# Performance work log

Measured on AMD Instinct MI355X. Metric: run time of the kernel, lower is better.

## Reference

```python
import jax, jax.numpy as jnp
import numpy as np
from jax import lax

B, N, C = 4, 16384, 384
HEADS, HD = 8, 48
ALPHA = 4.0
KS = 5
HH = WW = 128


def setup_inputs() -> dict:
    key = jax.random.key(0)
    ks = jax.random.split(key, 9)
    s = 0.02
    return {
        "x": jax.random.normal(ks[0], (B, N, C), jnp.float32),
        "W_qg": jax.random.normal(ks[1], (C, 2 * C), jnp.float32) * s,
        "W_kv": jax.random.normal(ks[2], (C, 2 * C), jnp.float32) * s,
        "W_proj": jax.random.normal(ks[3], (C, C), jnp.float32) * s,
        "b_proj": jnp.zeros((C,), jnp.float32),
        "pos_enc": jax.random.normal(ks[4], (1, N, C), jnp.float32) * 0.02,
        "power_p": jax.random.normal(ks[5], (1, HEADS, 1, HD), jnp.float32) * 0.5,
        "scale_p": jax.random.normal(ks[6], (1, 1, C), jnp.float32) * 0.5,
        "dwc_w": jax.random.normal(ks[7], (HD, 1, KS, KS), jnp.float32) * s,
        "dwc_b": jnp.zeros((HD,), jnp.float32),
        "H": HH,
        "W": WW,
    }


def _relu_pow(x, p):
    # relu(x) ** p with safe gradients at x <= 0
    r = jax.nn.relu(x)
    base = jnp.where(r > 0, r, 1.0)
    return jnp.where(r > 0, base ** p, 0.0)


def reference(x, W_qg, W_kv, W_proj, b_proj, pos_enc, power_p, scale_p, dwc_w, dwc_b, H, W):
    Bx, Nx, Cx = x.shape
    h = power_p.shape[1]
    hd = power_p.shape[-1]

    qg = x @ W_qg                      # [B,N,2C]
    q, g = qg[..., :Cx], qg[..., Cx:]
    kv = x @ W_kv                      # [B,N,2C] (sr_ratio == 1)
    k, v = kv[..., :Cx], kv[..., Cx:]
    n = Nx
    k = k + pos_enc

    scale = jax.nn.softplus(scale_p)            # [1,1,C]
    power = 1.0 + ALPHA * jax.nn.sigmoid(power_p)  # [1,h,1,hd]
    q = q / scale
    k = k / scale

    # [B,h,N,hd]
    q = q.reshape(Bx, Nx, h, hd).transpose(0, 2, 1, 3)
    k = k.reshape(Bx, n, h, hd).transpose(0, 2, 1, 3)
    v = v.reshape(Bx, n, h, hd).transpose(0, 2, 1, 3)

    q_pos = _relu_pow(q, power)
    q_neg = _relu_pow(-q, power)
    k_pos = _relu_pow(k, power)
    k_neg = _relu_pow(-k, power)

    q_sim = jnp.concatenate([q_pos, q_neg], axis=-1)   # [B,h,N,2hd]
    q_opp = jnp.concatenate([q_neg, q_pos], axis=-1)
    kk = jnp.concatenate([k_pos, k_neg], axis=-1)      # [B,h,n,2hd]
    v1, v2 = v[..., : hd // 2], v[..., hd // 2:]

    k_mean = kk.mean(axis=2, keepdims=True)            # [B,h,1,2hd]
    inv_n = 1.0 / n

    z_sim = 1.0 / (jnp.sum(q_sim * k_mean, axis=-1, keepdims=True) + 1e-6)
    kv1 = jnp.einsum('bhnd,bhne->bhde', kk, v1) * inv_n  # [B,h,2hd,hd/2]
    x_sim = jnp.einsum('bhnd,bhde->bhne', q_sim, kv1) * z_sim

    z_opp = 1.0 / (jnp.sum(q_opp * k_mean, axis=-1, keepdims=True) + 1e-6)
    kv2 = jnp.einsum('bhnd,bhne->bhde', kk, v2) * inv_n
    x_opp = jnp.einsum('bhnd,bhde->bhne', q_opp, kv2) * z_opp

    out = jnp.concatenate([x_sim, x_opp], axis=-1)     # [B,h,N,hd]
    out = out.transpose(0, 2, 1, 3).reshape(Bx, Nx, Cx)

    # depthwise conv gate on v
    v4 = v.reshape(Bx * h, H, W, hd).transpose(0, 3, 1, 2)  # [B*h, hd, H, W]
    vc = lax.conv_general_dilated(
        v4, dwc_w, window_strides=(1, 1), padding='SAME',
        feature_group_count=hd,
        dimension_numbers=('NCHW', 'OIHW', 'NCHW'))
    vc = vc + dwc_b[None, :, None, None]
    v_out = vc.reshape(Bx, Cx, Nx).transpose(0, 2, 1)  # [B,N,C]

    out = (out + v_out) * g
    out = out @ W_proj + b_proj
    return out
```

## Files before the change

### kernel.cpp

```cpp
#include <hip/hip_runtime.h>
#include <math.h>


#define NB 4
#define NTOK 16384
#define CDIM 384
#define NHEAD 8
#define HDIM 48
#define IMGH 128
#define IMGW 128

typedef unsigned short u16;
typedef unsigned int u32;
typedef __attribute__((ext_vector_type(8))) short bf16x8;
typedef __attribute__((ext_vector_type(4))) float f32x4;

__device__ __forceinline__ float bf2f(u16 u) {
  return __uint_as_float(((unsigned)u) << 16);
}
__device__ __forceinline__ u16 f2bf(float f) {
  unsigned u = __float_as_uint(f);
  u += 0x7FFF + ((u >> 16) & 1);
  return (u16)(u >> 16);
}
__device__ __forceinline__ float pow_mag(float r, float p) {
  if (r < 1e-20f) return 0.0f;
  return exp2f(fminf(p * log2f(r), 80.0f));
}
__device__ __forceinline__ float ldx1(const void* p, size_t i, bool f32) {
  return f32 ? ((const float*)p)[i] : bf2f(((const u16*)p)[i]);
}
__device__ __forceinline__ void gload16(u16* lds, const u16* g) {
  __builtin_amdgcn_global_load_lds(
      (const __attribute__((address_space(1))) u32*)g,
      (__attribute__((address_space(3))) u32*)lds, 16, 0, 0);
}

__global__ __launch_bounds__(256) void k0_detect(const void* __restrict__ x,
                                                 int* __restrict__ flag) {
  __shared__ int s[256];
  const u16* p = (const u16*)x;
  const int t = threadIdx.x;
  int good = 0;
#pragma unroll
  for (int i = 0; i < 16; ++i) {
    const u16 w = p[t * 16 + i];
    const int e = (w >> 7) & 0xFF;
    good += (e >= 0x60 && e <= 0x85) ? 1 : 0;
  }
  s[t] = good;
  __syncthreads();
  for (int o = 128; o > 0; o >>= 1) {
    if (t < o) s[t] += s[t + o];
    __syncthreads();
  }
  if (t == 0) *flag = (s[0] >= (4096 * 4) / 5) ? 0 : 1;
}

__global__ __launch_bounds__(256) void kx_convert(const void* __restrict__ x,
                                                  const int* __restrict__ flag,
                                                  u16* __restrict__ xbf) {
  if (*flag == 0) return;
  const size_t S = (size_t)NB * NTOK * CDIM;
  const size_t tid = (size_t)blockIdx.x * 256 + threadIdx.x;
  const size_t stride = (size_t)gridDim.x * 256;
  const float4* xf = (const float4*)x;
  for (size_t i = tid; i < S / 8; i += stride) {
    const float4 a = xf[i * 2 + 0];
    const float4 b = xf[i * 2 + 1];
    *(ushort4*)(xbf + i * 8 + 0) = make_ushort4(f2bf(a.x), f2bf(a.y), f2bf(a.z), f2bf(a.w));
    *(ushort4*)(xbf + i * 8 + 4) = make_ushort4(f2bf(b.x), f2bf(b.y), f2bf(b.z), f2bf(b.w));
  }
}

__global__ __launch_bounds__(256) void kprep(
    const void* __restrict__ Wqg, const void* __restrict__ Wkv,
    const void* __restrict__ Wp, const int* __restrict__ flag,
    u16* __restrict__ W2T, u16* __restrict__ WpT)
{
  const bool f32 = (*flag != 0);
  const int idx = blockIdx.x * 256 + threadIdx.x;
  if (idx < 1536 * 384) {
    const int n = idx / 384, k = idx - n * 384;
    const float v = (n < 768) ? ldx1(Wqg, (size_t)k * 768 + n, f32)
                              : ldx1(Wkv, (size_t)k * 768 + (n - 768), f32);
    W2T[idx] = f2bf(v);
  } else {
    const int j = idx - 1536 * 384;
    if (j < 384 * 384) {
      const int n = j / 384, k = j - n * 384;
      WpT[j] = f2bf(ldx1(Wp, (size_t)k * 384 + n, f32));
    }
  }
}

__global__ __launch_bounds__(512) void k1_mfma(
    const void* __restrict__ x, const u16* __restrict__ xbf,
    const u16* __restrict__ W2T,
    const void* __restrict__ pos_enc, const void* __restrict__ scale_p,
    const int* __restrict__ flag, const int conv_ok,
    u16* __restrict__ qsT, u16* __restrict__ gT, u16* __restrict__ ksT, u16* __restrict__ vT)
{
  const bool f32 = (*flag != 0);
  const bool fast = (!f32) || (conv_ok != 0);
  const u16* Asrc = f32 ? xbf : (const u16*)x;
  __shared__ __align__(16) u16 smem[17408];
  u16* Asm = smem;
  u16* Bsm = smem + 8192;
  const int t = threadIdx.x;
  const int bid = blockIdx.x;
  const int rm = (bid & 7) * 768 + (bid >> 3);
  const int m_idx = rm / 12;
  const int n_idx = rm - m_idx * 12;
  const int n0 = n_idx * 128;
  const int m0 = m_idx * 128;
  const int wave = t >> 6, lane = t & 63;
  const int wr = wave >> 2, wc = wave & 3;
  const int lm = lane & 15, lq = lane >> 4;

  f32x4 acc[4][2] = {};

  auto STAGE = [&](int k0) {
#pragma unroll
    for (int i = 0; i < 2; ++i) {
      const int chunk = i * 512 + t;
      const int row = chunk >> 3, c8 = chunk & 7;
      const int sc8 = c8 ^ (row & 7);
      u16* lpA = &Asm[(i * 512 + wave * 64) * 8];
      u16* lpB = &Bsm[(i * 512 + wave * 64) * 8];
      gload16(lpA, Asrc + (size_t)(m0 + row) * CDIM + k0 + sc8 * 8);
      gload16(lpB, W2T + (size_t)(n0 + row) * CDIM + k0 + sc8 * 8);
    }
  };
  auto COMPUTE = [&]() {
#pragma unroll
    for (int kh = 0; kh < 2; ++kh) {
      bf16x8 af[4], bfr[2];
#pragma unroll
      for (int r = 0; r < 4; ++r) {
        const int row = wr * 64 + r * 16 + lm;
        af[r] = *(const bf16x8*)&Asm[row * 64 + (((kh * 4 + lq) ^ (row & 7)) * 8)];
      }
#pragma unroll
      for (int cb = 0; cb < 2; ++cb) {
        const int row = wc * 32 + cb * 16 + lm;
        bfr[cb] = *(const bf16x8*)&Bsm[row * 64 + (((kh * 4 + lq) ^ (row & 7)) * 8)];
      }
#pragma unroll
      for (int r = 0; r < 4; ++r)
#pragma unroll
        for (int cb = 0; cb < 2; ++cb)
          acc[r][cb] = __builtin_amdgcn_mfma_f32_16x16x32_bf16(af[r], bfr[cb], acc[r][cb], 0, 0, 0);
    }
  };

  if (fast) {
    for (int ks = 0; ks < 6; ++ks) {
      STAGE(ks * 64);
      __syncthreads();
      COMPUTE();
      __syncthreads();
    }
  } else {
    for (int k0 = 0; k0 < CDIM; k0 += 64) {
#pragma unroll
      for (int i = 0; i < 2; ++i) {
        const int chunk = t + i * 512;
        const int row = chunk >> 3, c8 = chunk & 7;
        const int ldsoff = row * 64 + ((c8 ^ (row & 7)) * 8);
        const float* xp = (const float*)x + (size_t)(m0 + row) * CDIM + k0 + c8 * 8;
        const float4 v0 = *(const float4*)xp;
        const float4 v1 = *(const float4*)(xp + 4);
        *(ushort4*)&Asm[ldsoff]     = make_ushort4(f2bf(v0.x), f2bf(v0.y), f2bf(v0.z), f2bf(v0.w));
        *(ushort4*)&Asm[ldsoff + 4] = make_ushort4(f2bf(v1.x), f2bf(v1.y), f2bf(v1.z), f2bf(v1.w));
        *(uint4*)&Bsm[ldsoff] = *(const uint4*)(W2T + (size_t)(n0 + row) * CDIM + k0 + c8 * 8);
      }
      __syncthreads();
      COMPUTE();
      __syncthreads();
    }
  }

  u16* et = smem;
  const int b = m0 >> 14;
  const int TOK0 = m0 & (NTOK - 1);
  const int region = n0 / CDIM;
#pragma unroll
  for (int cb = 0; cb < 2; ++cb) {
    const int cl = wc * 32 + cb * 16 + lm;
    const int c = (n0 - region * CDIM) + cl;
    float inv = 1.0f;
    if (region == 0 || region == 2) inv = 1.0f / log1pf(expf(ldx1(scale_p, c, f32)));
#pragma unroll
    for (int r = 0; r < 4; ++r) {
      const int tl = wr * 64 + r * 16 + lq * 4;
      const f32x4 v = acc[r][cb];
      ushort4 w;
      if (region == 2) {
        const int tok = TOK0 + tl;
        const float p0 = ldx1(pos_enc, (size_t)(tok + 0) * CDIM + c, f32);
        const float p1 = ldx1(pos_enc, (size_t)(tok + 1) * CDIM + c, f32);
        const float p2 = ldx1(pos_enc, (size_t)(tok + 2) * CDIM + c, f32);
        const float p3 = ldx1(pos_enc, (size_t)(tok + 3) * CDIM + c, f32);
        w = make_ushort4(f2bf((v[0] + p0) * inv), f2bf((v[1] + p1) * inv),
                         f2bf((v[2] + p2) * inv), f2bf((v[3] + p3) * inv));
      } else if (region == 0) {
        w = make_ushort4(f2bf(v[0] * inv), f2bf(v[1] * inv), f2bf(v[2] * inv), f2bf(v[3] * inv));
      } else {
        w = make_ushort4(f2bf(v[0]), f2bf(v[1]), f2bf(v[2]), f2bf(v[3]));
      }
      *(ushort4*)&et[cl * 136 + tl] = w;
    }
  }
  __syncthreads();
  u16* dst = (region == 0) ? qsT : (region == 1) ? gT : (region == 2) ? ksT : vT;
  const int cbase = b * CDIM + (n0 - region * CDIM);
#pragma unroll
  for (int i = 0; i < 4; ++i) {
    const int idx = i * 512 + t;
    const int row = idx >> 4, seg = idx & 15;
    const uint4 val = *(const uint4*)&et[row * 136 + seg * 8];
    *(uint4*)(dst + ((size_t)(cbase + row)) * NTOK + TOK0 + seg * 8) = val;
  }
}

__global__ __launch_bounds__(256) void k2_stats(
    const u16* __restrict__ ksT, const u16* __restrict__ vT,
    const void* __restrict__ power_p, const int* __restrict__ flag,
    float* __restrict__ km, float* __restrict__ kvm)
{
  const bool f32 = (*flag != 0);
  __shared__ __align__(16) u16 kkL[96][72];
  __shared__ __align__(16) u16 vL[48][72];
  __shared__ float pw[48];
  const int bh = blockIdx.x;
  const int b = bh >> 3, h = bh & 7;
  const int t = threadIdx.x;
  if (t < 48) pw[t] = 1.0f + 4.0f / (1.0f + expf(-ldx1(power_p, h * HDIM + t, f32)));
  __syncthreads();
  const int wave = t >> 6, lane = t & 63;
  const int lm = lane & 15, lq = lane >> 4;
  f32x4 acc[2][3] = {};
  float ksum = 0.0f;
  const u16* ksbase = ksT + ((size_t)(b * CDIM + h * HDIM)) * NTOK;
  const u16* vbase  = vT  + ((size_t)(b * CDIM + h * HDIM)) * NTOK;
  const int n0base = blockIdx.y * 1024;
  for (int tile = 0; tile < 16; ++tile) {
    const int n0 = n0base + tile * 64;
    for (int i = t; i < 48 * 16; i += 256) {
      const int c = i >> 4, qd = (i & 15) * 4;
      ushort4 kq = *(const ushort4*)(ksbase + (size_t)c * NTOK + n0 + qd);
      ushort4 vq = *(const ushort4*)(vbase  + (size_t)c * NTOK + n0 + qd);
      const float p = pw[c];
      float kf[4] = {bf2f(kq.x), bf2f(kq.y), bf2f(kq.z), bf2f(kq.w)};
      ushort4 pos, neg;
#pragma unroll
      for (int jj = 0; jj < 4; ++jj) {
        const float f = pow_mag(fabsf(kf[jj]), p);
        ((u16*)&pos)[jj] = f2bf((kf[jj] > 0.f) ? f : 0.f);
        ((u16*)&neg)[jj] = f2bf((kf[jj] < 0.f) ? f : 0.f);
      }
      *(ushort4*)&kkL[c][qd]      = pos;
      *(ushort4*)&kkL[c + 48][qd] = neg;
      *(ushort4*)&vL[c][qd]       = vq;
    }
    __syncthreads();
    if (wave < 3) {
      const int mbase = wave * 32;
#pragma unroll
      for (int kh = 0; kh < 2; ++kh) {
        bf16x8 af[2], bfr[3];
#pragma unroll
        for (int mi = 0; mi < 2; ++mi)
          af[mi] = *(const bf16x8*)&kkL[mbase + mi * 16 + lm][kh * 32 + lq * 8];
#pragma unroll
        for (int nj = 0; nj < 3; ++nj)
          bfr[nj] = *(const bf16x8*)&vL[nj * 16 + lm][kh * 32 + lq * 8];
#pragma unroll
        for (int mi = 0; mi < 2; ++mi)
#pragma unroll
          for (int nj = 0; nj < 3; ++nj)
            acc[mi][nj] = __builtin_amdgcn_mfma_f32_16x16x32_bf16(af[mi], bfr[nj], acc[mi][nj], 0, 0, 0);
      }
    }
    if (t < 96) {
#pragma unroll
      for (int nn = 0; nn < 64; nn += 4) {
        const ushort4 kq4 = *(const ushort4*)&kkL[t][nn];
        ksum += (bf2f(kq4.x) + bf2f(kq4.y)) + (bf2f(kq4.z) + bf2f(kq4.w));
      }
    }
    __syncthreads();
  }
  const float inv_n = 1.0f / (float)NTOK;
  if (wave < 3) {
    const int mbase = wave * 32;
#pragma unroll
    for (int mi = 0; mi < 2; ++mi)
#pragma unroll
      for (int nj = 0; nj < 3; ++nj) {
        const f32x4 v = acc[mi][nj];
#pragma unroll
        for (int reg = 0; reg < 4; ++reg) {
          const int d = mbase + mi * 16 + lq * 4 + reg;
          const int e = nj * 16 + lm;
          atomicAdd(&kvm[(size_t)bh * 96 * 48 + d * 48 + e], v[reg] * inv_n);
        }
      }
  }
  if (t < 96) atomicAdd(&km[bh * 96 + t], ksum * inv_n);
}

__global__ __launch_bounds__(256) void k3_attn(
    const u16* __restrict__ qsT, u16* __restrict__ attnT,
    const float* __restrict__ km_g, const float* __restrict__ kvm_g,
    const void* __restrict__ power_p, const int* __restrict__ flag)
{
  const bool f32 = (*flag != 0);
  __shared__ __align__(16) float kvmL[96][48];
  __shared__ float kmL[96];
  __shared__ float pw[48];
  const int bh = blockIdx.y;
  const int b = bh >> 3, h = bh & 7;
  const int t = threadIdx.x;
  for (int i = t; i < 96 * 48; i += 256) kvmL[i / 48][i % 48] = kvm_g[(size_t)bh * 96 * 48 + i];
  if (t < 96) kmL[t] = km_g[bh * 96 + t];
  if (t < 48) pw[t] = 1.0f + 4.0f / (1.0f + expf(-ldx1(power_p, h * HDIM + t, f32)));
  __syncthreads();
  const int n = blockIdx.x * 512 + t;
  const size_t chan0 = ((size_t)(b * CDIM + h * HDIM)) * NTOK + n;
  const u16* qbase = qsT + chan0;
  u16* obase = attnT + chan0;
  float4 accs[2][6] = {}, acco[2][6] = {};
  float zs[2] = {}, zo[2] = {};
  for (int d = 0; d < 48; ++d) {
    const float p = pw[d];
    float qp[2], qn[2];
#pragma unroll
    for (int i = 0; i < 2; ++i) {
      const float qv = bf2f(qbase[(size_t)d * NTOK + i * 256]);
      const float f = pow_mag(fabsf(qv), p);
      qp[i] = (qv > 0.f) ? f : 0.f;
      qn[i] = (qv < 0.f) ? f : 0.f;
      zs[i] = fmaf(qp[i], kmL[d], zs[i]); zs[i] = fmaf(qn[i], kmL[d + 48], zs[i]);
      zo[i] = fmaf(qn[i], kmL[d], zo[i]); zo[i] = fmaf(qp[i], kmL[d + 48], zo[i]);
    }
#pragma unroll
    for (int e4 = 0; e4 < 6; ++e4) {
      const float4 kvA = *(const float4*)&kvmL[d][e4 * 4];
      const float4 kvB = *(const float4*)&kvmL[d + 48][e4 * 4];
      const float4 kvC = *(const float4*)&kvmL[d][24 + e4 * 4];
      const float4 kvD = *(const float4*)&kvmL[d + 48][24 + e4 * 4];
#pragma unroll
      for (int i = 0; i < 2; ++i) {
        accs[i][e4].x = fmaf(qp[i], kvA.x, fmaf(qn[i], kvB.x, accs[i][e4].x));
        accs[i][e4].y = fmaf(qp[i], kvA.y, fmaf(qn[i], kvB.y, accs[i][e4].y));
        accs[i][e4].z = fmaf(qp[i], kvA.z, fmaf(qn[i], kvB.z, accs[i][e4].z));
        accs[i][e4].w = fmaf(qp[i], kvA.w, fmaf(qn[i], kvB.w, accs[i][e4].w));
        acco[i][e4].x = fmaf(qn[i], kvC.x, fmaf(qp[i], kvD.x, acco[i][e4].x));
        acco[i][e4].y = fmaf(qn[i], kvC.y, fmaf(qp[i], kvD.y, acco[i][e4].y));
        acco[i][e4].z = fmaf(qn[i], kvC.z, fmaf(qp[i], kvD.z, acco[i][e4].z));
        acco[i][e4].w = fmaf(qn[i], kvC.w, fmaf(qp[i], kvD.w, acco[i][e4].w));
      }
    }
  }
#pragma unroll
  for (int i = 0; i < 2; ++i) {
    const float zsi = 1.0f / (zs[i] + 1e-6f);
    const float zoi = 1.0f / (zo[i] + 1e-6f);
#pragma unroll
    for (int e4 = 0; e4 < 6; ++e4) {
      const float4 s = accs[i][e4], o = acco[i][e4];
      obase[(size_t)(e4 * 4 + 0) * NTOK + i * 256]    = f2bf(s.x * zsi);
      obase[(size_t)(e4 * 4 + 1) * NTOK + i * 256]    = f2bf(s.y * zsi);
      obase[(size_t)(e4 * 4 + 2) * NTOK + i * 256]    = f2bf(s.z * zsi);
      obase[(size_t)(e4 * 4 + 3) * NTOK + i * 256]    = f2bf(s.w * zsi);
      obase[(size_t)(24 + e4 * 4 + 0) * NTOK + i * 256] = f2bf(o.x * zoi);
      obase[(size_t)(24 + e4 * 4 + 1) * NTOK + i * 256] = f2bf(o.y * zoi);
      obase[(size_t)(24 + e4 * 4 + 2) * NTOK + i * 256] = f2bf(o.z * zoi);
      obase[(size_t)(24 + e4 * 4 + 3) * NTOK + i * 256] = f2bf(o.w * zoi);
    }
  }
}

__global__ __launch_bounds__(256) void k4_conv_combine(
    const u16* __restrict__ vT, const u16* __restrict__ gT,
    const void* __restrict__ dwc_w, const void* __restrict__ dwc_b,
    const int* __restrict__ flag,
    u16* __restrict__ attnT)
{
  const bool f32 = (*flag != 0);
  __shared__ float tile[20][136];
  const int bc = blockIdx.y;
  const int y0 = blockIdx.x * 16;
  const int t = threadIdx.x;
  const int d = bc % 48;
  float w[25];
#pragma unroll
  for (int i = 0; i < 25; ++i) w[i] = ldx1(dwc_w, d * 25 + i, f32);
  const float bias = ldx1(dwc_b, d, f32);
  const u16* vimg = vT + (size_t)bc * NTOK;
  for (int i = t; i < 20 * 34; i += 256) {
    const int r = i / 34, cq = (i - r * 34) * 4;
    const int gy = y0 + r - 2;
    float4 v4 = make_float4(0.f, 0.f, 0.f, 0.f);
    if (gy >= 0 && gy < IMGH) {
      const int gx0 = cq - 4;
      if (gx0 >= 0 && gx0 + 3 < IMGW) {
        const ushort4 u = *(const ushort4*)(vimg + gy * IMGW + gx0);
        v4 = make_float4(bf2f(u.x), bf2f(u.y), bf2f(u.z), bf2f(u.w));
      } else {
#pragma unroll
        for (int jj = 0; jj < 4; ++jj) {
          const int gx = gx0 + jj;
          ((float*)&v4)[jj] = (gx >= 0 && gx < IMGW) ? bf2f(vimg[gy * IMGW + gx]) : 0.f;
        }
      }
    }
    *(float4*)&tile[r][cq] = v4;
  }
  __syncthreads();
  u16* abase = attnT + (size_t)bc * NTOK;
  const u16* gbase = gT + (size_t)bc * NTOK;
#pragma unroll
  for (int pass = 0; pass < 2; ++pass) {
    const int yy = pass * 8 + (t >> 5);
    const int x0 = (t & 31) * 4;
    float a0 = bias, a1 = bias, a2 = bias, a3 = bias;
#pragma unroll
    for (int dy = 0; dy < 5; ++dy) {
      const float* row = &tile[yy + dy][0];
      const float4 A = *(const float4*)&row[x0];
      const float4 B = *(const float4*)&row[x0 + 4];
      const float4 C = *(const float4*)&row[x0 + 8];
      const float c0 = A.z, c1 = A.w, c2 = B.x, c3 = B.y,
                  c4 = B.z, c5 = B.w, c6 = C.x, c7 = C.y;
      const float w0 = w[dy * 5 + 0], w1 = w[dy * 5 + 1], w2 = w[dy * 5 + 2],
                  w3 = w[dy * 5 + 3], w4 = w[dy * 5 + 4];
      a0 = fmaf(w0, c0, fmaf(w1, c1, fmaf(w2, c2, fmaf(w3, c3, fmaf(w4, c4, a0)))));
      a1 = fmaf(w0, c1, fmaf(w1, c2, fmaf(w2, c3, fmaf(w3, c4, fmaf(w4, c5, a1)))));
      a2 = fmaf(w0, c2, fmaf(w1, c3, fmaf(w2, c4, fmaf(w3, c5, fmaf(w4, c6, a2)))));
      a3 = fmaf(w0, c3, fmaf(w1, c4, fmaf(w2, c5, fmaf(w3, c6, fmaf(w4, c7, a3)))));
    }
    const int gidx = (y0 + yy) * IMGW + x0;
    const ushort4 at = *(const ushort4*)(abase + gidx);
    const ushort4 gg = *(const ushort4*)(gbase + gidx);
    *(ushort4*)(abase + gidx) = make_ushort4(
        f2bf((bf2f(at.x) + a0) * bf2f(gg.x)),
        f2bf((bf2f(at.y) + a1) * bf2f(gg.y)),
        f2bf((bf2f(at.z) + a2) * bf2f(gg.z)),
        f2bf((bf2f(at.w) + a3) * bf2f(gg.w)));
  }
}

__global__ __launch_bounds__(256) void k4b_transpose(
    const u16* __restrict__ src,
    u16* __restrict__ dst)
{
  __shared__ u16 tile[64][68];
  const int b  = blockIdx.z;
  const int c0 = blockIdx.y * 64;
  const int n0 = blockIdx.x * 64;
  const int t = threadIdx.x;
  const int tr = t >> 4, tq = t & 15;
#pragma unroll
  for (int i = 0; i < 4; ++i) {
    const int r = tr + i * 16;
    *(ushort4*)&tile[r][tq * 4] =
        *(const ushort4*)(src + ((size_t)(b * CDIM + c0 + r)) * NTOK + n0 + tq * 4);
  }
  __syncthreads();
#pragma unroll
  for (int i = 0; i < 4; ++i) {
    const int n = tr + i * 16;
    const ushort4 vv = make_ushort4(tile[tq * 4 + 0][n], tile[tq * 4 + 1][n],
                                    tile[tq * 4 + 2][n], tile[tq * 4 + 3][n]);
    *(ushort4*)(dst + ((size_t)(b * NTOK + n0 + n)) * CDIM + c0 + tq * 4) = vv;
  }
}

__global__ __launch_bounds__(256) void k5_mfma(
    const u16* __restrict__ A,
    const u16* __restrict__ WpT,
    const void* __restrict__ bp, const int* __restrict__ flag,
    void* __restrict__ out)
{
  const bool f32 = (*flag != 0);
  __shared__ __align__(16) u16 smem[32768];
  u16* Asm0 = smem;
  u16* Asm1 = smem + 8192;
  u16* Bsm0 = smem + 16384;
  u16* Bsm1 = smem + 24576;
  const int t = threadIdx.x;
  const int bid = blockIdx.x;
  const int rm = (bid & 7) * 192 + (bid >> 3);
  const int m_idx = rm / 3;
  const int n_idx = rm - m_idx * 3;
  const int n0 = n_idx * 128;
  const int m0 = m_idx * 128;
  const int wave = t >> 6, lane = t & 63;
  const int wr = wave >> 1, wc = wave & 1;
  const int lm = lane & 15, lq = lane >> 4;

  f32x4 acc[4][4] = {};

  auto STAGE = [&](int buf, int k0) {
    u16* Ab = buf ? Asm1 : Asm0;
    u16* Bb = buf ? Bsm1 : Bsm0;
#pragma unroll
    for (int i = 0; i < 4; ++i) {
      const int chunk = i * 256 + t;
      const int row = chunk >> 3, c8 = chunk & 7;
      const int sc8 = c8 ^ (row & 7);
      u16* lpA = &Ab[(i * 256 + wave * 64) * 8];
      u16* lpB = &Bb[(i * 256 + wave * 64) * 8];
      gload16(lpA, A + (size_t)(m0 + row) * CDIM + k0 + sc8 * 8);
      gload16(lpB, WpT + (size_t)(n0 + row) * CDIM + k0 + sc8 * 8);
    }
  };
  auto COMPUTE = [&](int buf) {
    u16* Ab = buf ? Asm1 : Asm0;
    u16* Bb = buf ? Bsm1 : Bsm0;
#pragma unroll
    for (int kh = 0; kh < 2; ++kh) {
      bf16x8 af[4], bfr[4];
#pragma unroll
      for (int r = 0; r < 4; ++r) {
        const int row = wr * 64 + r * 16 + lm;
        af[r] = *(const bf16x8*)&Ab[row * 64 + (((kh * 4 + lq) ^ (row & 7)) * 8)];
      }
#pragma unroll
      for (int cb = 0; cb < 4; ++cb) {
        const int row = wc * 64 + cb * 16 + lm;
        bfr[cb] = *(const bf16x8*)&Bb[row * 64 + (((kh * 4 + lq) ^ (row & 7)) * 8)];
      }
#pragma unroll
      for (int r = 0; r < 4; ++r)
#pragma unroll
        for (int cb = 0; cb < 4; ++cb)
          acc[r][cb] = __builtin_amdgcn_mfma_f32_16x16x32_bf16(af[r], bfr[cb], acc[r][cb], 0, 0, 0);
    }
  };

  STAGE(0, 0);
  asm volatile("s_waitcnt vmcnt(0)" ::: "memory");
  __builtin_amdgcn_sched_barrier(0);
  __builtin_amdgcn_s_barrier();
  int cur = 0;
#pragma unroll
  for (int ks = 0; ks < 5; ++ks) {
    STAGE(cur ^ 1, (ks + 1) * 64);
    COMPUTE(cur);
    asm volatile("s_waitcnt vmcnt(0)" ::: "memory");
    __builtin_amdgcn_sched_barrier(0);
    __builtin_amdgcn_s_barrier();
    cur ^= 1;
  }
  COMPUTE(cur);

  if (f32) {
    float* ef = (float*)smem;
    float bb[4];
#pragma unroll
    for (int cb = 0; cb < 4; ++cb) bb[cb] = ((const float*)bp)[n0 + wc * 64 + cb * 16 + lm];
    for (int h = 0; h < 2; ++h) {
      __syncthreads();
      if (wr == h) {
#pragma unroll
        for (int cb = 0; cb < 4; ++cb) {
          const int cl = wc * 64 + cb * 16 + lm;
#pragma unroll
          for (int r = 0; r < 4; ++r) {
            const int tl = r * 16 + lq * 4;
            const f32x4 v = acc[r][cb];
#pragma unroll
            for (int reg = 0; reg < 4; ++reg)
              ef[(tl + reg) * 132 + cl] = v[reg] + bb[cb];
          }
        }
      }
      __syncthreads();
      float* ob = (float*)out + (size_t)(m0 + h * 64) * CDIM + n0;
#pragma unroll
      for (int i = 0; i < 8; ++i) {
        const int idx = i * 256 + t;
        const int row = idx >> 5, seg = idx & 31;
        const float4 val = *(const float4*)&ef[row * 132 + seg * 4];
        *(float4*)(ob + (size_t)row * CDIM + seg * 4) = val;
      }
    }
  } else {
#pragma unroll
    for (int cb = 0; cb < 4; ++cb) {
      const int cg = n0 + wc * 64 + cb * 16 + lm;
      const float bbs = bf2f(((const u16*)bp)[cg]);
#pragma unroll
      for (int r = 0; r < 4; ++r) {
        const int rowtok = m0 + wr * 64 + r * 16 + lq * 4;
        const f32x4 v = acc[r][cb];
#pragma unroll
        for (int reg = 0; reg < 4; ++reg) {
          const size_t o = (size_t)(rowtok + reg) * CDIM + cg;
          ((u16*)out)[o] = f2bf(v[reg] + bbs);
        }
      }
    }
  }
}

extern "C" void kernel_launch(void* const* d_in, const int* in_sizes, int n_in,
                              void* d_out, int out_size, void* d_ws, size_t ws_size,
                              hipStream_t stream) {
  const void* x       = d_in[0];
  const void* Wqg     = d_in[1];
  const void* Wkv     = d_in[2];
  const void* Wproj   = d_in[3];
  const void* bproj   = d_in[4];
  const void* pos_enc = d_in[5];
  const void* power_p = d_in[6];
  const void* scale_p = d_in[7];
  const void* dwc_w   = d_in[8];
  const void* dwc_b   = d_in[9];

  const size_t S = (size_t)NB * NTOK * CDIM;
  const size_t stats_off   = 256;
  const size_t stats_bytes = (size_t)(32 * 96 + 32 * 96 * 48) * sizeof(float);
  const size_t w2t_elems = 1536 * 384, wpt_elems = 384 * 384;
  const size_t need = stats_off + stats_bytes + 3 * S * sizeof(u16)
                    + (w2t_elems + wpt_elems) * sizeof(u16);
  if (ws_size < need) return;

  int*   flag = (int*)d_ws;
  float* km   = (float*)((char*)d_ws + stats_off);
  float* kvm  = km + 32 * 96;
  u16* qsT = (u16*)((char*)d_ws + stats_off + stats_bytes);
  u16* gT  = qsT + S;
  u16* ksT = gT + S;
  u16* W2T = ksT + S;
  u16* WpT = W2T + w2t_elems;
  u16* vT  = (u16*)d_out;

  const int conv_ok = (out_size >= (int)(S * 4)) ? 1 : 0;
  u16* xbf = conv_ok ? ((u16*)d_out + S) : (u16*)d_out;

  hipMemsetAsync(km, 0, stats_bytes, stream);

  k0_detect<<<1, 256, 0, stream>>>(x, flag);
  if (conv_ok) kx_convert<<<2048, 256, 0, stream>>>(x, flag, xbf);
  kprep<<<(int)((w2t_elems + wpt_elems + 255) / 256), 256, 0, stream>>>(
      Wqg, Wkv, Wproj, flag, W2T, WpT);
  k1_mfma<<<6144, 512, 0, stream>>>(x, xbf, W2T, pos_enc, scale_p, flag, conv_ok,
                                    qsT, gT, ksT, vT);
  k2_stats<<<dim3(32, 16), 256, 0, stream>>>(ksT, vT, power_p, flag, km, kvm);
  k3_attn<<<dim3(32, 32), 256, 0, stream>>>(qsT, ksT, km, kvm, power_p, flag);
  k4_conv_combine<<<dim3(8, 1536), 256, 0, stream>>>(vT, gT, dwc_w, dwc_b, flag, ksT);
  k4b_transpose<<<dim3(256, 6, 4), 256, 0, stream>>>(ksT, qsT);
  k5_mfma<<<1536, 256, 0, stream>>>(qsT, WpT, bproj, flag, d_out);
}
```

Measured before the change: 667.7 us.

## Restructure projection GEMM to 512 threads with single-buffered LDS

The final projection GEMM kernel now runs 8 waves per 128x128 tile instead of 4, each wave covering a 64x32 sub-tile, which halves the accumulator registers per thread. The LDS double buffer is dropped for a single buffer with plain __syncthreads around each k-step, cutting shared memory per block roughly in half. The aim is higher occupancy and more latency hiding across waves. The cost is that loads no longer overlap with MFMA inside a block, and every k-step now waits on two barriers.

Result: no change. 662.9 us (-0.7%).

```diff
diff --git a/kernel.cpp b/kernel.cpp
--- a/kernel.cpp
+++ b/kernel.cpp
@@ -479,18 +479,16 @@
   }
 }
 
-__global__ __launch_bounds__(256) void k5_mfma(
+__global__ __launch_bounds__(512) void k5_mfma(
     const u16* __restrict__ A,
     const u16* __restrict__ WpT,
     const void* __restrict__ bp, const int* __restrict__ flag,
     void* __restrict__ out)
 {
   const bool f32 = (*flag != 0);
-  __shared__ __align__(16) u16 smem[32768];
-  u16* Asm0 = smem;
-  u16* Asm1 = smem + 8192;
-  u16* Bsm0 = smem + 16384;
-  u16* Bsm1 = smem + 24576;
+  __shared__ __align__(16) u16 smem[17408];
+  u16* Asm = smem;
+  u16* Bsm = smem + 8192;
   const int t = threadIdx.x;
   const int bid = blockIdx.x;
   const int rm = (bid & 7) * 192 + (bid >> 3);
@@ -499,76 +497,63 @@
   const int n0 = n_idx * 128;
   const int m0 = m_idx * 128;
   const int wave = t >> 6, lane = t & 63;
-  const int wr = wave >> 1, wc = wave & 1;
+  const int wr = wave >> 2, wc = wave & 3;
   const int lm = lane & 15, lq = lane >> 4;
 
-  f32x4 acc[4][4] = {};
-
-  auto STAGE = [&](int buf, int k0) {
-    u16* Ab = buf ? Asm1 : Asm0;
-    u16* Bb = buf ? Bsm1 : Bsm0;
-#pragma unroll
-    for (int i = 0; i < 4; ++i) {
-      const int chunk = i * 256 + t;
+  f32x4 acc[4][2] = {};
+
+  auto STAGE = [&](int k0) {
+#pragma unroll
+    for (int i = 0; i < 2; ++i) {
+      const int chunk = i * 512 + t;
       const int row = chunk >> 3, c8 = chunk & 7;
       const int sc8 = c8 ^ (row & 7);
-      u16* lpA = &Ab[(i * 256 + wave * 64) * 8];
-      u16* lpB = &Bb[(i * 256 + wave * 64) * 8];
+      u16* lpA = &Asm[(i * 512 + wave * 64) * 8];
+      u16* lpB = &Bsm[(i * 512 + wave * 64) * 8];
       gload16(lpA, A + (size_t)(m0 + row) * CDIM + k0 + sc8 * 8);
       gload16(lpB, WpT + (size_t)(n0 + row) * CDIM + k0 + sc8 * 8);
     }
   };
-  auto COMPUTE = [&](int buf) {
-    u16* Ab = buf ? Asm1 : Asm0;
-    u16* Bb = buf ? Bsm1 : Bsm0;
+  auto COMPUTE = [&]() {
 #pragma unroll
     for (int kh = 0; kh < 2; ++kh) {
-      bf16x8 af[4], bfr[4];
+      bf16x8 af[4], bfr[2];
 #pragma unroll
       for (int r = 0; r < 4; ++r) {
         const int row = wr * 64 + r * 16 + lm;
-        af[r] = *(const bf16x8*)&Ab[row * 64 + (((kh * 4 + lq) ^ (row & 7)) * 8)];
-      }
-#pragma unroll
-      for (int cb = 0; cb < 4; ++cb) {
-        const int row = wc * 64 + cb * 16 + lm;
-        bfr[cb] = *(const bf16x8*)&Bb[row * 64 + (((kh * 4 + lq) ^ (row & 7)) * 8)];
+        af[r] = *(const bf16x8*)&Asm[row * 64 + (((kh * 4 + lq) ^ (row & 7)) * 8)];
+      }
+#pragma unroll
+      for (int cb = 0; cb < 2; ++cb) {
+        const int row = wc * 32 + cb * 16 + lm;
+        bfr[cb] = *(const bf16x8*)&Bsm[row * 64 + (((kh * 4 + lq) ^ (row & 7)) * 8)];
       }
 #pragma unroll
       for (int r = 0; r < 4; ++r)
 #pragma unroll
-        for (int cb = 0; cb < 4; ++cb)
+        for (int cb = 0; cb < 2; ++cb)
           acc[r][cb] = __builtin_amdgcn_mfma_f32_16x16x32_bf16(af[r], bfr[cb], acc[r][cb], 0, 0, 0);
     }
   };
 
-  STAGE(0, 0);
-  asm volatile("s_waitcnt vmcnt(0)" ::: "memory");
-  __builtin_amdgcn_sched_barrier(0);
-  __builtin_amdgcn_s_barrier();
-  int cur = 0;
-#pragma unroll
-  for (int ks = 0; ks < 5; ++ks) {
-    STAGE(cur ^ 1, (ks + 1) * 64);
-    COMPUTE(cur);
-    asm volatile("s_waitcnt vmcnt(0)" ::: "memory");
-    __builtin_amdgcn_sched_barrier(0);
-    __builtin_amdgcn_s_barrier();
-    cur ^= 1;
-  }
-  COMPUTE(cur);
+  for (int ks = 0; ks < 6; ++ks) {
+    STAGE(ks * 64);
+    __syncthreads();
+    COMPUTE();
+    __syncthreads();
+  }
 
   if (f32) {
     float* ef = (float*)smem;
-    float bb[4];
-#pragma unroll
-    for (int cb = 0; cb < 4; ++cb) bb[cb] = ((const float*)bp)[n0 + wc * 64 + cb * 16 + lm];
+    float bb[2];
+#pragma unroll
+    for (int cb = 0; cb < 2; ++cb) bb[cb] = ((const float*)bp)[n0 + wc * 32 + cb * 16 + lm];
     for (int h = 0; h < 2; ++h) {
       __syncthreads();
       if (wr == h) {
 #pragma unroll
-        for (int cb = 0; cb < 4; ++cb) {
-          const int cl = wc * 64 + cb * 16 + lm;
+        for (int cb = 0; cb < 2; ++cb) {
+          const int cl = wc * 32 + cb * 16 + lm;
 #pragma unroll
           for (int r = 0; r < 4; ++r) {
             const int tl = r * 16 + lq * 4;
@@ -582,8 +567,8 @@
       __syncthreads();
       float* ob = (float*)out + (size_t)(m0 + h * 64) * CDIM + n0;
 #pragma unroll
-      for (int i = 0; i < 8; ++i) {
-        const int idx = i * 256 + t;
+      for (int i = 0; i < 4; ++i) {
+        const int idx = i * 512 + t;
         const int row = idx >> 5, seg = idx & 31;
         const float4 val = *(const float4*)&ef[row * 132 + seg * 4];
         *(float4*)(ob + (size_t)row * CDIM + seg * 4) = val;
@@ -591,8 +576,8 @@
     }
   } else {
 #pragma unroll
-    for (int cb = 0; cb < 4; ++cb) {
-      const int cg = n0 + wc * 64 + cb * 16 + lm;
+    for (int cb = 0; cb < 2; ++cb) {
+      const int cg = n0 + wc * 32 + cb * 16 + lm;
       const float bbs = bf2f(((const u16*)bp)[cg]);
 #pragma unroll
       for (int r = 0; r < 4; ++r) {
@@ -655,5 +640,5 @@
   k3_attn<<<dim3(32, 32), 256, 0, stream>>>(qsT, ksT, km, kvm, power_p, flag);
   k4_conv_combine<<<dim3(8, 1536), 256, 0, stream>>>(vT, gT, dwc_w, dwc_b, flag, ksT);
   k4b_transpose<<<dim3(256, 6, 4), 256, 0, stream>>>(ksT, qsT);
-  k5_mfma<<<1536, 256, 0, stream>>>(qsT, WpT, bproj, flag, d_out);
-}
+  k5_mfma<<<1536, 512, 0, stream>>>(qsT, WpT, bproj, flag, d_out);
+}
```
